# Performance work log

Measured on AMD Instinct MI355X. Metric: run time of the kernel, lower is better.

Reference implementation:

```python
import jax, jax.numpy as jnp
import numpy as np

EPS = 1e-6


def setup_inputs() -> dict:
    key = jax.random.key(0)
    kx, kw = jax.random.split(key)
    B, C, N = 8, 256, 2048
    x = jax.random.normal(kx, (B, C, N), dtype=jnp.float32)
    # nn.Linear(dim*2, 2, bias=False): weight shape [2, 2*C]
    W = jax.random.normal(kw, (2, 2 * C), dtype=jnp.float32) * (1.0 / np.sqrt(2 * C))
    return {"x": x, "W": W}


def reference(x, W):
    B, C, N = x.shape
    # cosine similarity matrix [B, N, N]
    sim = jnp.einsum('bcn,bcm->bnm', x, x)
    # torch: sqrt(sum(x^2 + 1e-6, dim=1)) -> eps added per-channel before sum
    norms = jnp.sqrt(jnp.sum(x * x + EPS, axis=1))            # [B, N]
    io_abs = sim / (norms[:, :, None] * norms[:, None, :])    # [B, N, N]
    # zero the diagonal (fill_diagonal_(0)) before argmax
    io_abs = io_abs * (1.0 - jnp.eye(N, dtype=io_abs.dtype))
    idx = jnp.argmax(io_abs, axis=2)                          # [B, N] nearest-neighbor per token
    # gather retrieved features: f_re[b, :, n] = x[b, :, idx[b, n]]
    f_re = jnp.take_along_axis(x, idx[:, None, :], axis=2)    # [B, C, N]
    # gated fusion
    fus = jnp.concatenate([x, f_re], axis=1).transpose(0, 2, 1)  # [B, N, 2C]
    w = jax.nn.softmax(fus @ W.T, axis=-1)                    # [B, N, 2]
    w = w.transpose(0, 2, 1)                                  # [B, 2, N]
    out = x * w[:, 0:1, :] + f_re * w[:, 1:2, :]
    return (out, f_re)
```

## Files before the change

kernel.cpp:

```cpp
#include <hip/hip_runtime.h>
#include <hip/hip_bf16.h>
#include <math.h>

constexpr int B_ = 8;
constexpr int C_ = 256;
constexpr int N_ = 2048;
constexpr int CN_ = C_ * N_;
constexpr int TOT_ = B_ * C_ * N_;
constexpr int NTILES = 16;
constexpr int NPAIRS = 136;

typedef __attribute__((ext_vector_type(8))) short bf16x8;
typedef __attribute__((ext_vector_type(4))) float f32x4;

__device__ __forceinline__ void g2l16(const void* g, void* l) {
    __builtin_amdgcn_global_load_lds(
        (const __attribute__((address_space(1))) void*)g,
        (__attribute__((address_space(3))) void*)l, 16, 0, 0);
}

__device__ __forceinline__ unsigned short bits(__hip_bfloat16 h) {
    union { __hip_bfloat16 b; unsigned short u; } cv;
    cv.b = h;
    return cv.u;
}

__device__ __forceinline__ float b2f(short s) {
    union { float f; unsigned u; } cv;
    cv.u = ((unsigned)(unsigned short)s) << 16;
    return cv.f;
}

__device__ __forceinline__ unsigned long long packkey(float v, int m) {
    const unsigned b = __float_as_uint(v);
    const unsigned u = (b & 0x80000000u) ? ~b : (b | 0x80000000u);
    return ((unsigned long long)u << 32) | (unsigned)(2047 - m);
}

__global__ __launch_bounds__(256) void convert_kernel(const float* __restrict__ x,
                                                      __hip_bfloat16* __restrict__ hiT,
                                                      __hip_bfloat16* __restrict__ loT,
                                                      float* __restrict__ normacc) {
    const int blk = blockIdx.x;
    const int batch = blk & 7;
    const int nt = (blk >> 3) & 31;
    const int ctile = blk >> 8;
    const int n0 = nt << 6, c0 = ctile << 6;
    const int t = threadIdx.x;
    const int i = t & 63, j = t >> 6;

    __shared__ float tb[64][65];
    __shared__ float red[4][64];

    float s = 0.f;
    const float* xp = x + (size_t)batch * CN_ + (size_t)c0 * N_ + n0 + i;
#pragma unroll 4
    for (int r = 0; r < 16; ++r) {
        const int cl = j + r * 4;
        const float v = xp[(size_t)cl * N_];
        tb[cl][i] = v;
        s += v * v;
    }
    red[j][i] = s;
    __syncthreads();

    const int cp = t & 31;
    const int c2 = cp << 1;
    const int nb = t >> 5;
#pragma unroll 4
    for (int r = 0; r < 8; ++r) {
        const int n = nb + r * 8;
        const float v0 = tb[c2][n], v1 = tb[c2 + 1][n];
        const size_t o = ((size_t)batch * N_ + n0 + n) * C_ + c0 + c2;
        const __hip_bfloat16 h0 = __float2bfloat16(v0);
        const __hip_bfloat16 h1 = __float2bfloat16(v1);
        const __hip_bfloat16 g0 = __float2bfloat16(v0 - __bfloat162float(h0));
        const __hip_bfloat16 g1 = __float2bfloat16(v1 - __bfloat162float(h1));
        ((unsigned*)hiT)[o >> 1] = ((unsigned)bits(h1) << 16) | bits(h0);
        ((unsigned*)loT)[o >> 1] = ((unsigned)bits(g1) << 16) | bits(g0);
    }
    if (j == 0) {
        const float tt = red[0][i] + red[1][i] + red[2][i] + red[3][i];
        atomicAdd(normacc + batch * N_ + n0 + i, tt);
    }
}

__global__ void rnorm_fin_kernel(const float* __restrict__ normacc,
                                 float* __restrict__ rnorm) {
    const int t = blockIdx.x * 256 + threadIdx.x;
    rnorm[t] = 1.0f / sqrtf(normacc[t] + 256.0f * 1e-6f);
}

__global__ __launch_bounds__(512) void gram_mfma_kernel(
        const __hip_bfloat16* __restrict__ hiT, const __hip_bfloat16* __restrict__ loT,
        const float* __restrict__ rnorm,
        float* __restrict__ pval, int* __restrict__ pidx, float* __restrict__ pval2) {
    const int blk = blockIdx.x;
    const int batch = blk & 7;
    int p = blk >> 3;
    int bn = 0;
    while (p >= NTILES - bn) { p -= NTILES - bn; ++bn; }
    const int bm = bn + p;
    const bool diag = (bn == bm);
    const int n0 = bn << 7, m0 = bm << 7;

    __shared__ short As0[128 * 64];
    __shared__ short As1[128 * 64];
    __shared__ short Bs0[128 * 64];
    __shared__ short Bs1[128 * 64];
    short* ov = &As0[0];
    float (*rv1)[4] = (float(*)[4])(ov + 0);
    int (*ri1)[4] = (int(*)[4])(ov + 1024);
    float (*rv2)[4] = (float(*)[4])(ov + 2048);
    float (*cv1)[2] = (float(*)[2])(ov + 3072);
    int (*ci1)[2] = (int(*)[2])(ov + 3584);
    float (*cv2)[2] = (float(*)[2])(ov + 4096);
    float* rnA = (float*)(ov + 4608);

    const int tid = threadIdx.x;
    const int l = tid & 63, w = tid >> 6;
    const int lm = l & 15, q = l >> 4;
    const int x7 = lm & 7;
    const int wn = (w >> 2) << 6;
    const int wm = (w & 3) << 5;

    const size_t bbase = (size_t)batch * CN_;
    const short* gA[2];
    const short* gB[2];
    int ldsoff[2];
#pragma unroll
    for (int pp = 0; pp < 2; ++pp) {
        const int slot = tid + pp * 512;
        const int r = slot >> 3, sidx = slot & 7;
        const int sw = sidx ^ (r & 7);
        const short* base = (const short*)((sw < 4) ? hiT : loT);
        gA[pp] = base + bbase + (size_t)(n0 + r) * C_ + (sw & 3) * 8;
        gB[pp] = base + bbase + (size_t)(m0 + r) * C_ + (sw & 3) * 8;
        ldsoff[pp] = slot * 8;
    }
    int aoff[8], boff[4];
#pragma unroll
    for (int rt = 0; rt < 4; ++rt) {
        const int ra = wn + rt * 16 + lm;
        aoff[rt * 2] = ra * 64 + ((q ^ x7) * 8);
        aoff[rt * 2 + 1] = ra * 64 + (((4 | q) ^ x7) * 8);
    }
#pragma unroll
    for (int ct = 0; ct < 2; ++ct) {
        const int rb = wm + ct * 16 + lm;
        boff[ct * 2] = rb * 64 + ((q ^ x7) * 8);
        boff[ct * 2 + 1] = rb * 64 + (((4 | q) ^ x7) * 8);
    }

    f32x4 acc[4][2];
#pragma unroll
    for (int rt = 0; rt < 4; ++rt)
#pragma unroll
        for (int ct = 0; ct < 2; ++ct) acc[rt][ct] = (f32x4){0.f, 0.f, 0.f, 0.f};

#pragma unroll
    for (int pp = 0; pp < 2; ++pp) {
        g2l16(gA[pp], As0 + ldsoff[pp]);
        g2l16(gB[pp], Bs0 + ldsoff[pp]);
    }
    __syncthreads();

#pragma unroll
    for (int kt = 0; kt < 8; ++kt) {
        short* Ac = (kt & 1) ? As1 : As0;
        short* Bc = (kt & 1) ? Bs1 : Bs0;
        if (kt < 7) {
            short* An = (kt & 1) ? As0 : As1;
            short* Bn = (kt & 1) ? Bs0 : Bs1;
#pragma unroll
            for (int pp = 0; pp < 2; ++pp) {
                g2l16(gA[pp] + (kt + 1) * 32, An + ldsoff[pp]);
                g2l16(gB[pp] + (kt + 1) * 32, Bn + ldsoff[pp]);
            }
        }
        bf16x8 ah[4], al[4], bh[2], bl[2];
#pragma unroll
        for (int rt = 0; rt < 4; ++rt) {
            ah[rt] = *(const bf16x8*)(Ac + aoff[rt * 2]);
            al[rt] = *(const bf16x8*)(Ac + aoff[rt * 2 + 1]);
        }
#pragma unroll
        for (int ct = 0; ct < 2; ++ct) {
            bh[ct] = *(const bf16x8*)(Bc + boff[ct * 2]);
            bl[ct] = *(const bf16x8*)(Bc + boff[ct * 2 + 1]);
        }
#pragma unroll
        for (int rt = 0; rt < 4; ++rt)
#pragma unroll
            for (int ct = 0; ct < 2; ++ct) {
                acc[rt][ct] = __builtin_amdgcn_mfma_f32_16x16x32_bf16(
                    ah[rt], bh[ct], acc[rt][ct], 0, 0, 0);
                acc[rt][ct] = __builtin_amdgcn_mfma_f32_16x16x32_bf16(
                    ah[rt], bl[ct], acc[rt][ct], 0, 0, 0);
                acc[rt][ct] = __builtin_amdgcn_mfma_f32_16x16x32_bf16(
                    al[rt], bh[ct], acc[rt][ct], 0, 0, 0);
            }
        __syncthreads();
    }

    if (tid < 128) rnA[tid] = rnorm[batch * N_ + n0 + tid];

    float rnm[2];
#pragma unroll
    for (int ct = 0; ct < 2; ++ct) rnm[ct] = rnorm[batch * N_ + m0 + wm + ct * 16 + lm];

#pragma unroll
    for (int rt = 0; rt < 4; ++rt) {
#pragma unroll
        for (int r = 0; r < 4; ++r) {
            const int nrow = n0 + wn + rt * 16 + q * 4 + r;
            float v1 = -3.4e38f, v2 = -3.4e38f;
            int i1 = 0x7fffffff;
#pragma unroll
            for (int ct = 0; ct < 2; ++ct) {
                const int m = m0 + wm + ct * 16 + lm;
                const float v = acc[rt][ct][r] * rnm[ct];
                if (m == nrow) continue;
                if (v > v1) { v2 = v1; v1 = v; i1 = m; }
                else if (v > v2) v2 = v;
            }
#pragma unroll
            for (int d = 1; d < 16; d <<= 1) {
                const float ov1 = __shfl_xor(v1, d, 64);
                const int oi1 = __shfl_xor(i1, d, 64);
                const float ov2 = __shfl_xor(v2, d, 64);
                if (ov1 > v1 || (ov1 == v1 && oi1 < i1)) {
                    v2 = fmaxf(v1, ov2); v1 = ov1; i1 = oi1;
                } else {
                    v2 = fmaxf(v2, ov1);
                }
            }
            if (lm == 0) {
                const int rloc = wn + rt * 16 + q * 4 + r;
                rv1[rloc][w & 3] = v1;
                ri1[rloc][w & 3] = i1;
                rv2[rloc][w & 3] = v2;
            }
        }
    }
    __syncthreads();

    if (!diag) {
        float rnn[4][4];
#pragma unroll
        for (int rt = 0; rt < 4; ++rt)
#pragma unroll
            for (int r = 0; r < 4; ++r) rnn[rt][r] = rnA[wn + rt * 16 + q * 4 + r];
#pragma unroll
        for (int ct = 0; ct < 2; ++ct) {
            float v1 = -3.4e38f, v2 = -3.4e38f;
            int i1 = 0x7fffffff;
#pragma unroll
            for (int rt = 0; rt < 4; ++rt) {
#pragma unroll
                for (int r = 0; r < 4; ++r) {
                    const float v = acc[rt][ct][r] * rnn[rt][r];
                    const int nn = n0 + wn + rt * 16 + q * 4 + r;
                    if (v > v1) { v2 = v1; v1 = v; i1 = nn; }
                    else if (v > v2) v2 = v;
                }
            }
#pragma unroll
            for (int d = 16; d < 64; d <<= 1) {
                const float ov1 = __shfl_xor(v1, d, 64);
                const int oi1 = __shfl_xor(i1, d, 64);
                const float ov2 = __shfl_xor(v2, d, 64);
                if (ov1 > v1 || (ov1 == v1 && oi1 < i1)) {
                    v2 = fmaxf(v1, ov2); v1 = ov1; i1 = oi1;
                } else {
                    v2 = fmaxf(v2, ov1);
                }
            }
            if (q == 0) {
                const int mloc = wm + ct * 16 + lm;
                cv1[mloc][w >> 2] = v1;
                ci1[mloc][w >> 2] = i1;
                cv2[mloc][w >> 2] = v2;
            }
        }
    }
    __syncthreads();

    if (tid < 128) {
        {
            float v1 = rv1[tid][0]; int i1 = ri1[tid][0]; float v2 = rv2[tid][0];
#pragma unroll
            for (int s = 1; s < 4; ++s) {
                const float ov1 = rv1[tid][s]; const int oi1 = ri1[tid][s]; const float ov2 = rv2[tid][s];
                if (ov1 > v1 || (ov1 == v1 && oi1 < i1)) { v2 = fmaxf(v1, ov2); v1 = ov1; i1 = oi1; }
                else v2 = fmaxf(v2, ov1);
            }
            const size_t gi = (size_t)(batch * NTILES + bm) * N_ + n0 + tid;
            pval[gi] = v1; pidx[gi] = i1; pval2[gi] = v2;
        }
        if (!diag) {
            float v1 = cv1[tid][0]; int i1 = ci1[tid][0]; float v2 = cv2[tid][0];
            const float ov1 = cv1[tid][1]; const int oi1 = ci1[tid][1]; const float ov2 = cv2[tid][1];
            if (ov1 > v1 || (ov1 == v1 && oi1 < i1)) { v2 = fmaxf(v1, ov2); v1 = ov1; i1 = oi1; }
            else v2 = fmaxf(v2, ov1);
            const size_t gi = (size_t)(batch * NTILES + bn) * N_ + m0 + tid;
            pval[gi] = v1; pidx[gi] = i1; pval2[gi] = v2;
        }
    }
}

__global__ void combine_kernel(const float* __restrict__ pval, const int* __restrict__ pidx,
                               const float* __restrict__ pval2, int* __restrict__ fidx,
                               int* __restrict__ rcnt, int* __restrict__ ridx,
                               unsigned long long* __restrict__ pbest) {
    const int t = blockIdx.x * 256 + threadIdx.x;
    const int batch = t >> 11, n = t & 2047;
    float v1 = -3.4e38f, v2 = -3.4e38f;
    int i1 = 0x7fffffff;
    for (int s = 0; s < NTILES; ++s) {
        const size_t gi = (size_t)(batch * NTILES + s) * N_ + n;
        const float ov1 = pval[gi]; const int oi1 = pidx[gi]; const float ov2 = pval2[gi];
        if (ov1 > v1 || (ov1 == v1 && oi1 < i1)) { v2 = fmaxf(v1, ov2); v1 = ov1; i1 = oi1; }
        else v2 = fmaxf(v2, ov1);
    }
    fidx[t] = i1;
    if (v1 - v2 < 1e-4f) {
        const int slot = atomicAdd(rcnt, 1);
        ridx[slot] = t;
        pbest[slot] = 0ull;
    }
}

__global__ __launch_bounds__(256) void rescue_kernel(const float* __restrict__ x,
                                                     const float* __restrict__ rnorm,
                                                     const int* __restrict__ rcnt,
                                                     const int* __restrict__ ridx,
                                                     unsigned long long* __restrict__ pbest) {
    const int cnt = *rcnt;
    const int nwork = cnt << 3;
    const int tid = threadIdx.x;
    __shared__ unsigned long long bk[256];
    for (int wi = blockIdx.x; wi < nwork; wi += gridDim.x) {
        const int rr = wi >> 3, ch = wi & 7;
        const int t = ridx[rr];
        const int batch = t >> 11, n = t & 2047;
        const int m = (ch << 8) + tid;
        const float* xb = x + (size_t)batch * CN_;
        float s0 = 0.f, s1 = 0.f, s2 = 0.f, s3 = 0.f;
        const float* xn = xb + n;
        const float* xm = xb + m;
#pragma unroll 4
        for (int c = 0; c < C_; c += 4) {
            s0 += xn[(size_t)(c + 0) * N_] * xm[(size_t)(c + 0) * N_];
            s1 += xn[(size_t)(c + 1) * N_] * xm[(size_t)(c + 1) * N_];
            s2 += xn[(size_t)(c + 2) * N_] * xm[(size_t)(c + 2) * N_];
            s3 += xn[(size_t)(c + 3) * N_] * xm[(size_t)(c + 3) * N_];
        }
        const float v = ((s0 + s1) + (s2 + s3)) * rnorm[batch * N_ + m];
        bk[tid] = (m == n) ? 0ull : packkey(v, m);
        __syncthreads();
        for (int sft = 128; sft > 0; sft >>= 1) {
            if (tid < sft) {
                const unsigned long long o = bk[tid + sft];
                if (o > bk[tid]) bk[tid] = o;
            }
            __syncthreads();
        }
        if (tid == 0) atomicMax(&pbest[rr], bk[0]);
        __syncthreads();
    }
}

__global__ void rescue_fin_kernel(const unsigned long long* __restrict__ pbest,
                                  const int* __restrict__ rcnt,
                                  const int* __restrict__ ridx,
                                  int* __restrict__ fidx) {
    const int rr = blockIdx.x * 256 + threadIdx.x;
    if (rr < *rcnt) {
        const unsigned long long k = pbest[rr];
        const int m = 2047 - (int)(unsigned)(k & 0xffffffffull);
        fidx[ridx[rr]] = m;
    }
}

__global__ __launch_bounds__(256) void finish_kernel(const float* __restrict__ x,
                                                     const __hip_bfloat16* __restrict__ hiT,
                                                     const __hip_bfloat16* __restrict__ loT,
                                                     const float* __restrict__ W,
                                                     const int* __restrict__ fidx,
                                                     float* __restrict__ out) {
    const int batch = blockIdx.x & 7;
    const int nt = blockIdx.x >> 3;
    const int n0 = nt << 4;
    const int t = threadIdx.x;
    const int i = t & 15, cg = t >> 4;

    __shared__ float Wl[1024];
    __shared__ int il[16];
    __shared__ float l0r[16][17], l1r[16][17];
    __shared__ float w0s[16], w1s[16];

    for (int u = t; u < 1024; u += 256) Wl[u] = W[u];
    if (t < 16) il[t] = fidx[batch * N_ + n0 + t];
    __syncthreads();

    const float* xb = x + (size_t)batch * CN_ + n0 + i;
    const int myidx = il[i];
    const size_t row = ((size_t)batch * N_ + myidx) * C_ + cg * 16;

    float fvv[16];
    {
        const bf16x8* hp = (const bf16x8*)(hiT + row);
        const bf16x8* lp = (const bf16x8*)(loT + row);
#pragma unroll
        for (int v8 = 0; v8 < 2; ++v8) {
            const bf16x8 h = hp[v8];
            const bf16x8 g = lp[v8];
#pragma unroll
            for (int e = 0; e < 8; ++e) fvv[v8 * 8 + e] = b2f(h[e]) + b2f(g[e]);
        }
    }

    float l0 = 0.f, l1 = 0.f;
#pragma unroll
    for (int cc = 0; cc < 16; ++cc) {
        const int c = cg * 16 + cc;
        const float xv = xb[(size_t)c * N_];
        l0 += xv * Wl[c] + fvv[cc] * Wl[256 + c];
        l1 += xv * Wl[512 + c] + fvv[cc] * Wl[768 + c];
    }
    l0r[cg][i] = l0;
    l1r[cg][i] = l1;
    __syncthreads();
    if (t < 16) {
        float L0 = 0.f, L1 = 0.f;
#pragma unroll
        for (int g = 0; g < 16; ++g) { L0 += l0r[g][t]; L1 += l1r[g][t]; }
        const float mx = fmaxf(L0, L1);
        const float e0 = expf(L0 - mx);
        const float e1 = expf(L1 - mx);
        const float inv = 1.0f / (e0 + e1);
        w0s[t] = e0 * inv;
        w1s[t] = e1 * inv;
    }
    __syncthreads();
    const float w0 = w0s[i], w1 = w1s[i];

#pragma unroll
    for (int cc = 0; cc < 16; ++cc) {
        const int c = cg * 16 + cc;
        const size_t off = (size_t)batch * CN_ + (size_t)c * N_ + n0 + i;
        const float xv = xb[(size_t)c * N_];
        out[off] = xv * w0 + fvv[cc] * w1;
        out[TOT_ + off] = fvv[cc];
    }
}

extern "C" void kernel_launch(void* const* d_in, const int* in_sizes, int n_in,
                              void* d_out, int out_size, void* d_ws, size_t ws_size,
                              hipStream_t stream) {
    const float* x = (const float*)d_in[0];
    const float* W = (const float*)d_in[1];
    float* out = (float*)d_out;

    const size_t BF_BYTES = (size_t)TOT_ * 2;
    const size_t NORM_BYTES = (size_t)B_ * N_ * 4;
    const size_t P_BYTES = (size_t)B_ * NTILES * N_ * 4;

    uint8_t* p = (uint8_t*)d_ws;
    __hip_bfloat16* hiT = (__hip_bfloat16*)p; p += BF_BYTES;
    __hip_bfloat16* loT = (__hip_bfloat16*)p; p += BF_BYTES;
    float* rnorm = (float*)p; p += NORM_BYTES;
    float* normacc = (float*)p; p += NORM_BYTES;
    float* pval = (float*)p; p += P_BYTES;
    int* pidx = (int*)p; p += P_BYTES;
    float* pval2 = (float*)p; p += P_BYTES;
    int* fidx = (int*)p; p += NORM_BYTES;
    int* rcnt = (int*)p; p += 256;
    int* ridx = (int*)p; p += NORM_BYTES;
    unsigned long long* pbest = (unsigned long long*)p; p += (size_t)B_ * N_ * 8;

    hipMemsetAsync(rcnt, 0, 4, stream);
    hipMemsetAsync(normacc, 0, NORM_BYTES, stream);
    convert_kernel<<<1024, 256, 0, stream>>>(x, hiT, loT, normacc);
    rnorm_fin_kernel<<<64, 256, 0, stream>>>(normacc, rnorm);
    gram_mfma_kernel<<<B_ * NPAIRS, 512, 0, stream>>>(hiT, loT, rnorm, pval, pidx, pval2);
    combine_kernel<<<64, 256, 0, stream>>>(pval, pidx, pval2, fidx, rcnt, ridx, pbest);
    rescue_kernel<<<256, 256, 0, stream>>>(x, rnorm, rcnt, ridx, pbest);
    rescue_fin_kernel<<<64, 256, 0, stream>>>(pbest, rcnt, ridx, fidx);
    finish_kernel<<<1024, 256, 0, stream>>>(x, hiT, loT, W, fidx, out);
}
```

Baseline: 180.0 us.

## Single-buffer gram LDS, inline rnorm, retile finish kernel

Removes the separate rnorm kernel and computes reciprocal norms inline from the accumulated sums in the gram and rescue kernels. The gram kernel drops its LDS double buffering for a single buffer with two barriers per k-step and requests higher occupancy through launch bounds. The finish kernel processes 64 tokens per 512-thread block and keeps x in registers instead of reloading it. These changes trade load/compute overlap and register headroom (spill risk) for occupancy and fewer launches.

```diff
diff --git a/kernel.cpp b/kernel.cpp
--- a/kernel.cpp
+++ b/kernel.cpp
@@ -9,6 +9,7 @@
 constexpr int TOT_ = B_ * C_ * N_;
 constexpr int NTILES = 16;
 constexpr int NPAIRS = 136;
+constexpr float EPSC = 256.0f * 1e-6f;
 
 typedef __attribute__((ext_vector_type(8))) short bf16x8;
 typedef __attribute__((ext_vector_type(4))) float f32x4;
@@ -85,15 +86,9 @@
     }
 }
 
-__global__ void rnorm_fin_kernel(const float* __restrict__ normacc,
-                                 float* __restrict__ rnorm) {
-    const int t = blockIdx.x * 256 + threadIdx.x;
-    rnorm[t] = 1.0f / sqrtf(normacc[t] + 256.0f * 1e-6f);
-}
-
-__global__ __launch_bounds__(512) void gram_mfma_kernel(
+__global__ __launch_bounds__(512, 8) void gram_mfma_kernel(
         const __hip_bfloat16* __restrict__ hiT, const __hip_bfloat16* __restrict__ loT,
-        const float* __restrict__ rnorm,
+        const float* __restrict__ normacc,
         float* __restrict__ pval, int* __restrict__ pidx, float* __restrict__ pval2) {
     const int blk = blockIdx.x;
     const int batch = blk & 7;
@@ -104,11 +99,9 @@
     const bool diag = (bn == bm);
     const int n0 = bn << 7, m0 = bm << 7;
 
-    __shared__ short As0[128 * 64];
-    __shared__ short As1[128 * 64];
-    __shared__ short Bs0[128 * 64];
-    __shared__ short Bs1[128 * 64];
-    short* ov = &As0[0];
+    __shared__ short As[128 * 64];
+    __shared__ short Bs[128 * 64];
+    short* ov = &As[0];
     float (*rv1)[4] = (float(*)[4])(ov + 0);
     int (*ri1)[4] = (int(*)[4])(ov + 1024);
     float (*rv2)[4] = (float(*)[4])(ov + 2048);
@@ -158,36 +151,24 @@
 #pragma unroll
         for (int ct = 0; ct < 2; ++ct) acc[rt][ct] = (f32x4){0.f, 0.f, 0.f, 0.f};
 
-#pragma unroll
-    for (int pp = 0; pp < 2; ++pp) {
-        g2l16(gA[pp], As0 + ldsoff[pp]);
-        g2l16(gB[pp], Bs0 + ldsoff[pp]);
-    }
-    __syncthreads();
-
-#pragma unroll
     for (int kt = 0; kt < 8; ++kt) {
-        short* Ac = (kt & 1) ? As1 : As0;
-        short* Bc = (kt & 1) ? Bs1 : Bs0;
-        if (kt < 7) {
-            short* An = (kt & 1) ? As0 : As1;
-            short* Bn = (kt & 1) ? Bs0 : Bs1;
-#pragma unroll
-            for (int pp = 0; pp < 2; ++pp) {
-                g2l16(gA[pp] + (kt + 1) * 32, An + ldsoff[pp]);
-                g2l16(gB[pp] + (kt + 1) * 32, Bn + ldsoff[pp]);
-            }
-        }
+        __syncthreads();
+#pragma unroll
+        for (int pp = 0; pp < 2; ++pp) {
+            g2l16(gA[pp] + kt * 32, As + ldsoff[pp]);
+            g2l16(gB[pp] + kt * 32, Bs + ldsoff[pp]);
+        }
+        __syncthreads();
         bf16x8 ah[4], al[4], bh[2], bl[2];
 #pragma unroll
         for (int rt = 0; rt < 4; ++rt) {
-            ah[rt] = *(const bf16x8*)(Ac + aoff[rt * 2]);
-            al[rt] = *(const bf16x8*)(Ac + aoff[rt * 2 + 1]);
+            ah[rt] = *(const bf16x8*)(As + aoff[rt * 2]);
+            al[rt] = *(const bf16x8*)(As + aoff[rt * 2 + 1]);
         }
 #pragma unroll
         for (int ct = 0; ct < 2; ++ct) {
-            bh[ct] = *(const bf16x8*)(Bc + boff[ct * 2]);
-            bl[ct] = *(const bf16x8*)(Bc + boff[ct * 2 + 1]);
+            bh[ct] = *(const bf16x8*)(Bs + boff[ct * 2]);
+            bl[ct] = *(const bf16x8*)(Bs + boff[ct * 2 + 1]);
         }
 #pragma unroll
         for (int rt = 0; rt < 4; ++rt)
@@ -200,14 +181,15 @@
                 acc[rt][ct] = __builtin_amdgcn_mfma_f32_16x16x32_bf16(
                     al[rt], bh[ct], acc[rt][ct], 0, 0, 0);
             }
-        __syncthreads();
-    }
-
-    if (tid < 128) rnA[tid] = rnorm[batch * N_ + n0 + tid];
+    }
+    __syncthreads();
+
+    if (tid < 128) rnA[tid] = 1.0f / sqrtf(normacc[batch * N_ + n0 + tid] + EPSC);
 
     float rnm[2];
 #pragma unroll
-    for (int ct = 0; ct < 2; ++ct) rnm[ct] = rnorm[batch * N_ + m0 + wm + ct * 16 + lm];
+    for (int ct = 0; ct < 2; ++ct)
+        rnm[ct] = 1.0f / sqrtf(normacc[batch * N_ + m0 + wm + ct * 16 + lm] + EPSC);
 
 #pragma unroll
     for (int rt = 0; rt < 4; ++rt) {
@@ -332,7 +314,7 @@
 }
 
 __global__ __launch_bounds__(256) void rescue_kernel(const float* __restrict__ x,
-                                                     const float* __restrict__ rnorm,
+                                                     const float* __restrict__ normacc,
                                                      const int* __restrict__ rcnt,
                                                      const int* __restrict__ ridx,
                                                      unsigned long long* __restrict__ pbest) {
@@ -356,7 +338,8 @@
             s2 += xn[(size_t)(c + 2) * N_] * xm[(size_t)(c + 2) * N_];
             s3 += xn[(size_t)(c + 3) * N_] * xm[(size_t)(c + 3) * N_];
         }
-        const float v = ((s0 + s1) + (s2 + s3)) * rnorm[batch * N_ + m];
+        const float rn = 1.0f / sqrtf(normacc[batch * N_ + m] + EPSC);
+        const float v = ((s0 + s1) + (s2 + s3)) * rn;
         bk[tid] = (m == n) ? 0ull : packkey(v, m);
         __syncthreads();
         for (int sft = 128; sft > 0; sft >>= 1) {
@@ -383,7 +366,7 @@
     }
 }
 
-__global__ __launch_bounds__(256) void finish_kernel(const float* __restrict__ x,
+__global__ __launch_bounds__(512) void finish_kernel(const float* __restrict__ x,
                                                      const __hip_bfloat16* __restrict__ hiT,
                                                      const __hip_bfloat16* __restrict__ loT,
                                                      const float* __restrict__ W,
@@ -391,51 +374,53 @@
                                                      float* __restrict__ out) {
     const int batch = blockIdx.x & 7;
     const int nt = blockIdx.x >> 3;
-    const int n0 = nt << 4;
+    const int n0 = nt << 6;
     const int t = threadIdx.x;
-    const int i = t & 15, cg = t >> 4;
+    const int lane = t & 63, cw = t >> 6;
 
     __shared__ float Wl[1024];
-    __shared__ int il[16];
-    __shared__ float l0r[16][17], l1r[16][17];
-    __shared__ float w0s[16], w1s[16];
-
-    for (int u = t; u < 1024; u += 256) Wl[u] = W[u];
-    if (t < 16) il[t] = fidx[batch * N_ + n0 + t];
-    __syncthreads();
-
-    const float* xb = x + (size_t)batch * CN_ + n0 + i;
-    const int myidx = il[i];
-    const size_t row = ((size_t)batch * N_ + myidx) * C_ + cg * 16;
-
-    float fvv[16];
+    __shared__ int il[64];
+    __shared__ float pl0[8][64], pl1[8][64];
+    __shared__ float w0s[64], w1s[64];
+
+    for (int u = t; u < 1024; u += 512) Wl[u] = W[u];
+    if (t < 64) il[t] = fidx[batch * N_ + n0 + t];
+    __syncthreads();
+
+    const int myrow = il[lane];
+    const size_t rowb = ((size_t)batch * N_ + myrow) * C_ + cw * 32;
+
+    float fre[32];
     {
-        const bf16x8* hp = (const bf16x8*)(hiT + row);
-        const bf16x8* lp = (const bf16x8*)(loT + row);
-#pragma unroll
-        for (int v8 = 0; v8 < 2; ++v8) {
+        const bf16x8* hp = (const bf16x8*)(hiT + rowb);
+        const bf16x8* lp = (const bf16x8*)(loT + rowb);
+#pragma unroll
+        for (int v8 = 0; v8 < 4; ++v8) {
             const bf16x8 h = hp[v8];
             const bf16x8 g = lp[v8];
 #pragma unroll
-            for (int e = 0; e < 8; ++e) fvv[v8 * 8 + e] = b2f(h[e]) + b2f(g[e]);
-        }
-    }
-
+            for (int e = 0; e < 8; ++e) fre[v8 * 8 + e] = b2f(h[e]) + b2f(g[e]);
+        }
+    }
+
+    const float* xb = x + (size_t)batch * CN_ + n0 + lane;
+    float xr[32];
     float l0 = 0.f, l1 = 0.f;
 #pragma unroll
-    for (int cc = 0; cc < 16; ++cc) {
-        const int c = cg * 16 + cc;
+    for (int cc = 0; cc < 32; ++cc) {
+        const int c = cw * 32 + cc;
         const float xv = xb[(size_t)c * N_];
-        l0 += xv * Wl[c] + fvv[cc] * Wl[256 + c];
-        l1 += xv * Wl[512 + c] + fvv[cc] * Wl[768 + c];
-    }
-    l0r[cg][i] = l0;
-    l1r[cg][i] = l1;
-    __syncthreads();
-    if (t < 16) {
+        xr[cc] = xv;
+        l0 += xv * Wl[c] + fre[cc] * Wl[256 + c];
+        l1 += xv * Wl[512 + c] + fre[cc] * Wl[768 + c];
+    }
+    pl0[cw][lane] = l0;
+    pl1[cw][lane] = l1;
+    __syncthreads();
+    if (t < 64) {
         float L0 = 0.f, L1 = 0.f;
 #pragma unroll
-        for (int g = 0; g < 16; ++g) { L0 += l0r[g][t]; L1 += l1r[g][t]; }
+        for (int g = 0; g < 8; ++g) { L0 += pl0[g][t]; L1 += pl1[g][t]; }
         const float mx = fmaxf(L0, L1);
         const float e0 = expf(L0 - mx);
         const float e1 = expf(L1 - mx);
@@ -444,15 +429,14 @@
         w1s[t] = e1 * inv;
     }
     __syncthreads();
-    const float w0 = w0s[i], w1 = w1s[i];
-
-#pragma unroll
-    for (int cc = 0; cc < 16; ++cc) {
-        const int c = cg * 16 + cc;
-        const size_t off = (size_t)batch * CN_ + (size_t)c * N_ + n0 + i;
-        const float xv = xb[(size_t)c * N_];
-        out[off] = xv * w0 + fvv[cc] * w1;
-        out[TOT_ + off] = fvv[cc];
+    const float w0 = w0s[lane], w1 = w1s[lane];
+
+#pragma unroll
+    for (int cc = 0; cc < 32; ++cc) {
+        const int c = cw * 32 + cc;
+        const size_t off = (size_t)batch * CN_ + (size_t)c * N_ + n0 + lane;
+        out[off] = xr[cc] * w0 + fre[cc] * w1;
+        out[TOT_ + off] = fre[cc];
     }
 }
 
@@ -470,7 +454,6 @@
     uint8_t* p = (uint8_t*)d_ws;
     __hip_bfloat16* hiT = (__hip_bfloat16*)p; p += BF_BYTES;
     __hip_bfloat16* loT = (__hip_bfloat16*)p; p += BF_BYTES;
-    float* rnorm = (float*)p; p += NORM_BYTES;
     float* normacc = (float*)p; p += NORM_BYTES;
     float* pval = (float*)p; p += P_BYTES;
     int* pidx = (int*)p; p += P_BYTES;
@@ -483,10 +466,9 @@
     hipMemsetAsync(rcnt, 0, 4, stream);
     hipMemsetAsync(normacc, 0, NORM_BYTES, stream);
     convert_kernel<<<1024, 256, 0, stream>>>(x, hiT, loT, normacc);
-    rnorm_fin_kernel<<<64, 256, 0, stream>>>(normacc, rnorm);
-    gram_mfma_kernel<<<B_ * NPAIRS, 512, 0, stream>>>(hiT, loT, rnorm, pval, pidx, pval2);
+    gram_mfma_kernel<<<B_ * NPAIRS, 512, 0, stream>>>(hiT, loT, normacc, pval, pidx, pval2);
     combine_kernel<<<64, 256, 0, stream>>>(pval, pidx, pval2, fidx, rcnt, ridx, pbest);
-    rescue_kernel<<<256, 256, 0, stream>>>(x, rnorm, rcnt, ridx, pbest);
+    rescue_kernel<<<256, 256, 0, stream>>>(x, normacc, rcnt, ridx, pbest);
     rescue_fin_kernel<<<64, 256, 0, stream>>>(pbest, rcnt, ridx, fidx);
-    finish_kernel<<<1024, 256, 0, stream>>>(x, hiT, loT, W, fidx, out);
-}
+    finish_kernel<<<256, 512, 0, stream>>>(x, hiT, loT, W, fidx, out);
+}
```

Result: slower. 193.6 us (+7.5%).
